# Optimization experiments

Hardware: AMD Instinct MI355X
Metric: run time of the kernel (lower is better)

## Reference

```python
import jax, jax.numpy as jnp
import numpy as np
import math

B, T, E, H = 64, 256, 1024, 16
HD = E // H  # 64
EPS = 1e-5


def layernorm(x, g, b):
    mu = jnp.mean(x, axis=-1, keepdims=True)
    var = jnp.mean(jnp.square(x - mu), axis=-1, keepdims=True)
    return (x - mu) * jax.lax.rsqrt(var + EPS) * g + b


def setup_inputs() -> dict:
    key = jax.random.key(0)
    ks = jax.random.split(key, 10)
    s = 0.02
    return {
        "x": jax.random.normal(ks[0], (B, T, E), dtype=jnp.float32),
        "ln1_g": jnp.ones((E,), jnp.float32),
        "ln1_b": jnp.zeros((E,), jnp.float32),
        "wk": jax.random.normal(ks[1], (H, E, HD), jnp.float32) * s,
        "wq": jax.random.normal(ks[2], (H, E, HD), jnp.float32) * s,
        "wv": jax.random.normal(ks[3], (H, E, HD), jnp.float32) * s,
        "w_proj": jax.random.normal(ks[4], (E, E), jnp.float32) * s,
        "b_proj": jnp.zeros((E,), jnp.float32),
        "ln2_g": jnp.ones((E,), jnp.float32),
        "ln2_b": jnp.zeros((E,), jnp.float32),
        "w1": jax.random.normal(ks[5], (E, E), jnp.float32) * s,
        "b1": jnp.zeros((E,), jnp.float32),
        "w2": jax.random.normal(ks[6], (E, E), jnp.float32) * s,
        "b2": jnp.zeros((E,), jnp.float32),
    }


def reference(x, ln1_g, ln1_b, wk, wq, wv, w_proj, b_proj, ln2_g, ln2_b, w1, b1, w2, b2):
    # --- multi-head causal attention on LN1(x) ---
    h = layernorm(x, ln1_g, ln1_b)
    k = jnp.einsum('bte,hed->bhtd', h, wk)
    q = jnp.einsum('bte,hed->bhtd', h, wq)
    v = jnp.einsum('bte,hed->bhtd', h, wv)
    # NOTE: original computes k @ q^T (K.Q^T), not the standard Q.K^T -- kept faithful
    scores = jnp.einsum('bhtd,bhsd->bhts', k, q) / math.sqrt(HD)
    mask = jnp.tril(jnp.ones((T, T), dtype=bool))
    scores = jnp.where(mask, scores, -jnp.inf)
    attn_w = jax.nn.softmax(scores, axis=-1)  # dropout = identity in eval
    attn = jnp.einsum('bhts,bhsd->bhtd', attn_w, v)
    attn = attn.transpose(0, 2, 1, 3).reshape(B, T, E)  # concat heads
    x = x + attn @ w_proj + b_proj
    # --- feed-forward on LN2(x) ---
    h2 = layernorm(x, ln2_g, ln2_b)
    ff = jax.nn.relu(h2 @ w1 + b1) @ w2 + b2
    return x + ff
```

## Files before the change

kernel.cpp:

```cpp
#include <hip/hip_runtime.h>

typedef unsigned int u32;
typedef unsigned short u16;
typedef __attribute__((ext_vector_type(8))) short bf16x8;
typedef __attribute__((ext_vector_type(4))) float f32x4;

#define GLOBAL_AS __attribute__((address_space(1)))
#define LDS_AS    __attribute__((address_space(3)))

#define B_   64
#define T_   256
#define E_   1024
#define H_   16
#define HD_  64
#define NTOK (B_*T_)
#define K_   1024
#define LNEPS 1e-5f

__device__ __forceinline__ float bflo(u32 u){ return __uint_as_float(u << 16); }
__device__ __forceinline__ float bfhi(u32 u){ return __uint_as_float(u & 0xffff0000u); }
__device__ __forceinline__ u16 f2bf(float f){
  u32 x = __float_as_uint(f);
  u32 r = x + 0x7fffu + ((x >> 16) & 1u);
  return (u16)(r >> 16);
}
__device__ __forceinline__ u16 f2bf_trunc(float f){
  return (u16)(__float_as_uint(f) >> 16);
}
__device__ __forceinline__ u32 pack2(float a, float b){
  return (u32)f2bf(a) | ((u32)f2bf(b) << 16);
}

__device__ __forceinline__ void gload16(const u16* g, u16* l){
  __builtin_amdgcn_global_load_lds((const GLOBAL_AS void*)g, (LDS_AS void*)l, 16, 0, 0);
}

__global__ __launch_bounds__(256) void ln_bf16_kernel(
    const float* __restrict__ x, const float* __restrict__ g,
    const float* __restrict__ b, u16* __restrict__ o)
{
  int lane  = threadIdx.x & 63;
  int token = (blockIdx.x << 2) + (threadIdx.x >> 6);
  const float4* xr = (const float4*)(x + (size_t)token * E_);
  float4 v[4];
  float s = 0.f, ss = 0.f;
  #pragma unroll
  for (int i = 0; i < 4; ++i){
    v[i] = xr[lane + 64 * i];
    s += v[i].x + v[i].y + v[i].z + v[i].w;
    ss = fmaf(v[i].x, v[i].x, fmaf(v[i].y, v[i].y,
         fmaf(v[i].z, v[i].z, fmaf(v[i].w, v[i].w, ss))));
  }
  #pragma unroll
  for (int off = 32; off > 0; off >>= 1){
    s  += __shfl_xor(s,  off);
    ss += __shfl_xor(ss, off);
  }
  float mu   = s * (1.f / E_);
  float var  = ss * (1.f / E_) - mu * mu;
  float rstd = rsqrtf(var + LNEPS);
  const float4* gr = (const float4*)g;
  const float4* br = (const float4*)b;
  uint2* orow = (uint2*)(o + (size_t)token * E_);
  #pragma unroll
  for (int i = 0; i < 4; ++i){
    float4 gg = gr[lane + 64 * i], bb = br[lane + 64 * i];
    float y0 = (v[i].x - mu) * rstd * gg.x + bb.x;
    float y1 = (v[i].y - mu) * rstd * gg.y + bb.y;
    float y2 = (v[i].z - mu) * rstd * gg.z + bb.z;
    float y3 = (v[i].w - mu) * rstd * gg.w + bb.w;
    orow[lane + 64 * i] = make_uint2(pack2(y0, y1), pack2(y2, y3));
  }
}

__global__ __launch_bounds__(256) void convq_kernel(
    const float* __restrict__ wk, const float* __restrict__ wq,
    const float* __restrict__ wv, u16* __restrict__ o)
{
  __shared__ float tile[64 * 68];
  const int zh = blockIdx.x, z = zh >> 4, h = zh & 15;
  const int e0 = blockIdx.y << 6;
  const float* w = (z == 0 ? wk : z == 1 ? wq : wv) + (size_t)h * (E_ * HD_);
  const int t = threadIdx.x;
  {
    int er = t >> 2, d0 = (t & 3) << 4;
    const float4* src = (const float4*)(w + (size_t)(e0 + er) * HD_ + d0);
    #pragma unroll
    for (int i = 0; i < 4; ++i)
      *(float4*)(tile + er * 68 + d0 + 4 * i) = src[i];
  }
  __syncthreads();
  {
    int dr = t >> 2, ee = (t & 3) << 4;
    u32 wd[8];
    #pragma unroll
    for (int j = 0; j < 8; ++j)
      wd[j] = pack2(tile[(ee + 2*j) * 68 + dr], tile[(ee + 2*j + 1) * 68 + dr]);
    u16* dst = o + (size_t)(z * 1024 + h * 64 + dr) * K_ + e0 + ee;
    *(uint4*)(dst    ) = make_uint4(wd[0], wd[1], wd[2], wd[3]);
    *(uint4*)(dst + 8) = make_uint4(wd[4], wd[5], wd[6], wd[7]);
  }
}

__global__ __launch_bounds__(256) void convt_kernel(
    const float* __restrict__ w, u16* __restrict__ o)
{
  __shared__ float tile[64 * 68];
  const int n0 = blockIdx.x << 6, k0 = blockIdx.y << 6;
  const int t = threadIdx.x;
  {
    int kr = t >> 2, nn = (t & 3) << 4;
    const float4* src = (const float4*)(w + (size_t)(k0 + kr) * E_ + n0 + nn);
    #pragma unroll
    for (int i = 0; i < 4; ++i)
      *(float4*)(tile + kr * 68 + nn + 4 * i) = src[i];
  }
  __syncthreads();
  {
    int nr = t >> 2, kk = (t & 3) << 4;
    u32 wd[8];
    #pragma unroll
    for (int j = 0; j < 8; ++j)
      wd[j] = pack2(tile[(kk + 2*j) * 68 + nr], tile[(kk + 2*j + 1) * 68 + nr]);
    u16* dst = o + (size_t)(n0 + nr) * K_ + k0 + kk;
    *(uint4*)(dst    ) = make_uint4(wd[0], wd[1], wd[2], wd[3]);
    *(uint4*)(dst + 8) = make_uint4(wd[4], wd[5], wd[6], wd[7]);
  }
}

#define MF4(I, AV)                                                                 \
  acc[I][0] = __builtin_amdgcn_mfma_f32_16x16x32_bf16(AV, b0, acc[I][0], 0, 0, 0); \
  acc[I][1] = __builtin_amdgcn_mfma_f32_16x16x32_bf16(AV, b1, acc[I][1], 0, 0, 0); \
  acc[I][2] = __builtin_amdgcn_mfma_f32_16x16x32_bf16(AV, b2, acc[I][2], 0, 0, 0); \
  acc[I][3] = __builtin_amdgcn_mfma_f32_16x16x32_bf16(AV, b3, acc[I][3], 0, 0, 0);

#define MG_SLICE(SLOT, DSTSLOT, KOFF, DO_STAGE, VM)                           \
  {                                                                           \
    const u16* As_ = lds + (SLOT) * 16384;                                    \
    const u16* Bs_ = As_ + 8192;                                              \
    u16* dst_ = lds + (DSTSLOT) * 16384;                                      \
    bf16x8 b0 = *(const bf16x8*)(Bs_ + boff);                                 \
    bf16x8 b1 = *(const bf16x8*)(Bs_ + boff + 512);                           \
    bf16x8 b2 = *(const bf16x8*)(Bs_ + boff + 1024);                          \
    bf16x8 b3 = *(const bf16x8*)(Bs_ + boff + 1536);                          \
    bf16x8 a0 = *(const bf16x8*)(As_ + aoff);                                 \
    bf16x8 a1 = *(const bf16x8*)(As_ + aoff + 512);                           \
    bf16x8 a2 = *(const bf16x8*)(As_ + aoff + 1024);                          \
    bf16x8 a3 = *(const bf16x8*)(As_ + aoff + 1536);                          \
    if (DO_STAGE) {                                                           \
      gload16(Ag0 + (KOFF), dst_ + tid * 8);                                  \
      gload16(Ag1 + (KOFF), dst_ + 4096 + tid * 8);                           \
    }                                                                         \
    __builtin_amdgcn_s_barrier();                                             \
    asm volatile("s_waitcnt lgkmcnt(0)" ::: "memory");                        \
    __builtin_amdgcn_sched_barrier(0);                                        \
    __builtin_amdgcn_s_setprio(1);                                            \
    MF4(0, a0) MF4(1, a1) MF4(2, a2) MF4(3, a3)                               \
    __builtin_amdgcn_s_setprio(0);                                            \
    __builtin_amdgcn_s_barrier();                                             \
    asm volatile("" ::: "memory");                                            \
    a0 = *(const bf16x8*)(As_ + aoff + 2048);                                 \
    a1 = *(const bf16x8*)(As_ + aoff + 2560);                                 \
    a2 = *(const bf16x8*)(As_ + aoff + 3072);                                 \
    a3 = *(const bf16x8*)(As_ + aoff + 3584);                                 \
    if (DO_STAGE) {                                                           \
      gload16(Bg0 + (KOFF), dst_ + 8192 + tid * 8);                           \
      gload16(Bg1 + (KOFF), dst_ + 12288 + tid * 8);                          \
    }                                                                         \
    __builtin_amdgcn_s_barrier();                                             \
    asm volatile("s_waitcnt lgkmcnt(0)" ::: "memory");                        \
    __builtin_amdgcn_sched_barrier(0);                                        \
    __builtin_amdgcn_s_setprio(1);                                            \
    MF4(4, a0) MF4(5, a1) MF4(6, a2) MF4(7, a3)                               \
    __builtin_amdgcn_s_setprio(0);                                            \
    VM;                                                                       \
    __builtin_amdgcn_s_barrier();                                             \
    asm volatile("" ::: "memory");                                            \
  }

template<int MODE>
__global__ __launch_bounds__(512, 2) void mgemm_kernel(
    const u16* __restrict__ A, const u16* __restrict__ Bt,
    const float* __restrict__ bias, const float* __restrict__ resid,
    float* __restrict__ Cf, u16* __restrict__ Cb, u16* __restrict__ Cb2)
{
  __shared__ __align__(16) u16 lds[65536];

  const int tid = threadIdx.x, lane = tid & 63, wid = tid >> 6;
  const int wm = wid >> 2, wn = wid & 3;
  const int l15 = lane & 15, quad = lane >> 4;

  const int nwg = (int)(gridDim.x * gridDim.y);
  int wg = (int)(blockIdx.y * gridDim.x + blockIdx.x);
  wg = (wg & 7) * (nwg >> 3) + (wg >> 3);
  const int row0 = (wg & 63) << 8;
  const int col0 = (wg >> 6) << 8;

  const int srow = tid >> 2;
  const int slog = (tid & 3) ^ ((srow + (srow >> 2)) & 3);
  const u16* Ag0 = A  + (size_t)(row0 + srow) * K_ + slog * 8;
  const u16* Ag1 = Ag0 + (size_t)128 * K_;
  const u16* Bg0 = Bt + (size_t)(col0 + srow) * K_ + slog * 8;
  const u16* Bg1 = Bg0 + (size_t)128 * K_;

  const int cofs = ((quad ^ ((l15 + (l15 >> 2)) & 3)) << 3);
  const int aoff = (wm * 128 + l15) * 32 + cofs;
  const int boff = (wn * 64  + l15) * 32 + cofs;

  f32x4 acc[8][4];
  #pragma unroll
  for (int i = 0; i < 8; ++i)
    #pragma unroll
    for (int j = 0; j < 4; ++j)
      acc[i][j] = (f32x4){0.f, 0.f, 0.f, 0.f};

  #pragma unroll
  for (int t = 0; t < 3; ++t) {
    u16* dst = lds + t * 16384;
    gload16(Ag0 + t * 32, dst + tid * 8);
    gload16(Ag1 + t * 32, dst + 4096 + tid * 8);
    gload16(Bg0 + t * 32, dst + 8192 + tid * 8);
    gload16(Bg1 + t * 32, dst + 12288 + tid * 8);
  }
  asm volatile("s_waitcnt vmcnt(8)" ::: "memory");
  __builtin_amdgcn_s_barrier();
  asm volatile("" ::: "memory");

  #pragma unroll 1
  for (int s = 0; s < 29; ++s)
    MG_SLICE(s & 3, (s + 3) & 3, (s + 3) * 32, 1,
             asm volatile("s_waitcnt vmcnt(8)" ::: "memory"))
  MG_SLICE(1, 0, 0, 0, asm volatile("s_waitcnt vmcnt(4)" ::: "memory"))
  MG_SLICE(2, 0, 0, 0, asm volatile("s_waitcnt vmcnt(0)" ::: "memory"))
  MG_SLICE(3, 0, 0, 0, ((void)0))

  if (MODE == 1 || MODE == 3) {
    const int rbase = row0 + wm * 128;
    #pragma unroll
    for (int j = 0; j < 4; ++j) {
      const int n = col0 + wn * 64 + j * 16 + l15;
      const float bn = bias[n];
      #pragma unroll
      for (int i = 0; i < 8; ++i)
        #pragma unroll
        for (int r = 0; r < 4; ++r) {
          const int row = rbase + i * 16 + quad * 4 + r;
          const size_t idx = (size_t)row * E_ + n;
          float v = acc[i][j][r] + bn;
          if (MODE == 1) Cf[idx] = v + resid[idx];
          else           Cf[idx] = v + Cf[idx];
        }
    }
    return;
  }

  u16* ep = lds + wid * 8192;
  const int nb0 = col0 + wn * 64;

  if (MODE == 2) {
    #pragma unroll
    for (int j = 0; j < 4; ++j) {
      const float bn = bias[nb0 + j * 16 + l15];
      #pragma unroll
      for (int i = 0; i < 8; ++i)
        #pragma unroll
        for (int r = 0; r < 4; ++r)
          ep[(i*16 + quad*4 + r) * 64 + j*16 + l15] =
              f2bf(fmaxf(acc[i][j][r] + bn, 0.f));
    }
    __syncthreads();
    const int rbase = row0 + wm * 128;
    #pragma unroll
    for (int it = 0; it < 16; ++it) {
      const int tl = it * 8 + (lane >> 3), c = lane & 7;
      uint4 v = *(const uint4*)(ep + tl * 64 + c * 8);
      *(uint4*)(Cb + (size_t)(rbase + tl) * E_ + nb0 + c * 8) = v;
    }
    return;
  }

  const int z = nb0 >> 10, hh = (nb0 >> 6) & 15;
  const int rows0 = row0 + wm * 128;
  const int bb = rows0 >> 8, tb0 = rows0 & 255;
  if (z < 2) {
    #pragma unroll
    for (int i = 0; i < 8; ++i)
      #pragma unroll
      for (int j = 0; j < 4; ++j)
        #pragma unroll
        for (int r = 0; r < 4; ++r)
          ep[(i*16 + quad*4 + r) * 64 + j*16 + l15] = f2bf(acc[i][j][r]);
    __syncthreads();
    u16* out = (z == 0 ? Cb : Cb2) + ((size_t)(bb * H_ + hh) * T_ + tb0) * HD_;
    #pragma unroll
    for (int it = 0; it < 16; ++it) {
      const int tl = it * 8 + (lane >> 3), c = lane & 7;
      uint4 v = *(const uint4*)(ep + tl * 64 + c * 8);
      *(uint4*)(out + (size_t)tl * HD_ + c * 8) = v;
    }
  } else {
    #pragma unroll
    for (int i = 0; i < 8; ++i)
      #pragma unroll
      for (int j = 0; j < 4; ++j)
        #pragma unroll
        for (int r = 0; r < 4; ++r) {
          const int tl = i*16 + quad*4 + r, d = j*16 + l15;
          const int phys = (tl >> 3) ^ (d & 15);
          ep[d * 128 + phys * 8 + (tl & 7)] = f2bf(acc[i][j][r]);
        }
    __syncthreads();
    u16* out = (u16*)Cf + ((size_t)(bb * H_ + hh) * HD_) * T_;
    #pragma unroll
    for (int it = 0; it < 16; ++it) {
      const int d = it * 4 + (lane >> 4), c = lane & 15;
      const int phys = c ^ (d & 15);
      uint4 v = *(const uint4*)(ep + d * 128 + phys * 8);
      *(uint4*)(out + (size_t)d * T_ + tb0 + c * 8) = v;
    }
  }
}

__global__ __launch_bounds__(256) void fattn_kernel(
    const u16* __restrict__ kk_, const u16* __restrict__ qq_,
    const u16* __restrict__ vt_, u16* __restrict__ out)
{
  __shared__ __align__(16) u16 Pb[4][64 * 72];
  const int tid = threadIdx.x, lane = tid & 63, wv = tid >> 6;
  const int bh = blockIdx.x * 4 + wv;
  const int tblk = blockIdx.y;
  const int l15 = lane & 15, quad = lane >> 4;
  const u16* kb  = kk_ + (size_t)bh * (T_ * HD_);
  const u16* qb  = qq_ + (size_t)bh * (T_ * HD_);
  const u16* vtb = vt_ + (size_t)bh * (HD_ * T_);
  u16* Pw = Pb[wv];

  bf16x8 kf[4][2];
  #pragma unroll
  for (int i = 0; i < 4; ++i)
    #pragma unroll
    for (int c = 0; c < 2; ++c)
      kf[i][c] = *(const bf16x8*)(kb + (size_t)(tblk*64 + i*16 + l15) * HD_ + c*32 + quad*8);

  f32x4 o[4][4];
  float mrow[4][4], lrow[4][4];
  #pragma unroll
  for (int i = 0; i < 4; ++i) {
    #pragma unroll
    for (int j = 0; j < 4; ++j) o[i][j] = (f32x4){0.f, 0.f, 0.f, 0.f};
    #pragma unroll
    for (int r = 0; r < 4; ++r) { mrow[i][r] = -1e30f; lrow[i][r] = 0.f; }
  }

  for (int sb = 0; sb <= tblk; ++sb) {
    f32x4 S[4][4];
    #pragma unroll
    for (int j = 0; j < 4; ++j) {
      bf16x8 qf0 = *(const bf16x8*)(qb + (size_t)(sb*64 + j*16 + l15) * HD_ +      quad*8);
      bf16x8 qf1 = *(const bf16x8*)(qb + (size_t)(sb*64 + j*16 + l15) * HD_ + 32 + quad*8);
      #pragma unroll
      for (int i = 0; i < 4; ++i) {
        f32x4 t0 = __builtin_amdgcn_mfma_f32_16x16x32_bf16(kf[i][0], qf0,
                       (f32x4){0.f,0.f,0.f,0.f}, 0, 0, 0);
        S[i][j] = __builtin_amdgcn_mfma_f32_16x16x32_bf16(kf[i][1], qf1, t0, 0, 0, 0);
      }
    }
    #pragma unroll
    for (int i = 0; i < 4; ++i)
      #pragma unroll
      for (int j = 0; j < 4; ++j)
        #pragma unroll
        for (int r = 0; r < 4; ++r) {
          float val = S[i][j][r] * 0.125f;
          if (sb == tblk) {
            int tl = i*16 + quad*4 + r, sl = j*16 + l15;
            if (sl > tl) val = -1e30f;
          }
          S[i][j][r] = val;
        }
    #pragma unroll
    for (int i = 0; i < 4; ++i)
      #pragma unroll
      for (int r = 0; r < 4; ++r) {
        float mx = fmaxf(fmaxf(S[i][0][r], S[i][1][r]), fmaxf(S[i][2][r], S[i][3][r]));
        #pragma unroll
        for (int msk = 1; msk < 16; msk <<= 1) mx = fmaxf(mx, __shfl_xor(mx, msk));
        float mn = fmaxf(mrow[i][r], mx);
        float al = __expf(mrow[i][r] - mn);
        mrow[i][r] = mn;
        float sm = 0.f;
        #pragma unroll
        for (int j = 0; j < 4; ++j) {
          float p = __expf(S[i][j][r] - mn);
          S[i][j][r] = p;
          sm += p;
        }
        #pragma unroll
        for (int msk = 1; msk < 16; msk <<= 1) sm += __shfl_xor(sm, msk);
        lrow[i][r] = lrow[i][r] * al + sm;
        #pragma unroll
        for (int jd = 0; jd < 4; ++jd) o[i][jd][r] *= al;
      }
    #pragma unroll
    for (int i = 0; i < 4; ++i)
      #pragma unroll
      for (int j = 0; j < 4; ++j)
        #pragma unroll
        for (int r = 0; r < 4; ++r)
          Pw[(i*16 + quad*4 + r) * 72 + j*16 + l15] = f2bf_trunc(S[i][j][r]);
    __syncthreads();
    bf16x8 pf[4][2];
    #pragma unroll
    for (int i = 0; i < 4; ++i)
      #pragma unroll
      for (int c = 0; c < 2; ++c)
        pf[i][c] = *(const bf16x8*)(Pw + (i*16 + l15) * 72 + c*32 + quad*8);
    #pragma unroll
    for (int jd = 0; jd < 4; ++jd) {
      bf16x8 vf0 = *(const bf16x8*)(vtb + (size_t)(jd*16 + l15) * T_ + sb*64 +      quad*8);
      bf16x8 vf1 = *(const bf16x8*)(vtb + (size_t)(jd*16 + l15) * T_ + sb*64 + 32 + quad*8);
      #pragma unroll
      for (int i = 0; i < 4; ++i) {
        f32x4 t0 = __builtin_amdgcn_mfma_f32_16x16x32_bf16(pf[i][0], vf0, o[i][jd], 0, 0, 0);
        o[i][jd] = __builtin_amdgcn_mfma_f32_16x16x32_bf16(pf[i][1], vf1, t0, 0, 0, 0);
      }
    }
    __syncthreads();
  }

  #pragma unroll
  for (int i = 0; i < 4; ++i)
    #pragma unroll
    for (int r = 0; r < 4; ++r) {
      float inv = 1.0f / lrow[i][r];
      #pragma unroll
      for (int jd = 0; jd < 4; ++jd)
        Pw[(i*16 + quad*4 + r) * 72 + jd*16 + l15] = f2bf(o[i][jd][r] * inv);
    }
  __syncthreads();
  {
    const int b = bh >> 4, h = bh & 15;
    const uint4* pr = (const uint4*)(Pw + lane * 72);
    uint4* og = (uint4*)(out + ((size_t)(b * T_ + tblk*64 + lane)) * E_ + h * HD_);
    #pragma unroll
    for (int k = 0; k < 8; ++k) og[k] = pr[k];
  }
}

extern "C" void kernel_launch(void* const* d_in, const int* in_sizes, int n_in,
                              void* d_out, int out_size, void* d_ws, size_t ws_size,
                              hipStream_t stream) {
  const float* x     = (const float*)d_in[0];
  const float* ln1g  = (const float*)d_in[1];
  const float* ln1b  = (const float*)d_in[2];
  const float* wk    = (const float*)d_in[3];
  const float* wq    = (const float*)d_in[4];
  const float* wv    = (const float*)d_in[5];
  const float* wproj = (const float*)d_in[6];
  const float* bproj = (const float*)d_in[7];
  const float* ln2g  = (const float*)d_in[8];
  const float* ln2b  = (const float*)d_in[9];
  const float* w1    = (const float*)d_in[10];
  const float* b1    = (const float*)d_in[11];
  const float* w2    = (const float*)d_in[12];
  const float* b2    = (const float*)d_in[13];
  float* outp = (float*)d_out;

  char* ws = (char*)d_ws;
  const size_t MB = 1024 * 1024;
  u16* wqkvT  = (u16*)(ws);
  u16* wprojT = (u16*)(ws + 6 * MB);
  u16* w1T    = (u16*)(ws + 8 * MB);
  u16* w2T    = (u16*)(ws + 10 * MB);
  u16* hb     = (u16*)(ws + 16 * MB);
  u16* kbuf   = (u16*)(ws + 48 * MB);
  u16* qbuf   = (u16*)(ws + 80 * MB);
  u16* vtbuf  = (u16*)d_out;

  convq_kernel<<<dim3(48, 16), 256, 0, stream>>>(wk, wq, wv, wqkvT);
  convt_kernel<<<dim3(16, 16), 256, 0, stream>>>(wproj, wprojT);
  convt_kernel<<<dim3(16, 16), 256, 0, stream>>>(w1, w1T);
  convt_kernel<<<dim3(16, 16), 256, 0, stream>>>(w2, w2T);

  ln_bf16_kernel<<<NTOK/4, 256, 0, stream>>>(x, ln1g, ln1b, hb);
  mgemm_kernel<0><<<dim3(64, 12), 512, 0, stream>>>(
      hb, wqkvT, nullptr, nullptr, (float*)vtbuf, kbuf, qbuf);
  fattn_kernel<<<dim3(B_*H_/4, 4), 256, 0, stream>>>(kbuf, qbuf, vtbuf, hb);
  mgemm_kernel<1><<<dim3(64, 4), 512, 0, stream>>>(
      hb, wprojT, bproj, x, outp, nullptr, nullptr);
  ln_bf16_kernel<<<NTOK/4, 256, 0, stream>>>(outp, ln2g, ln2b, kbuf);
  mgemm_kernel<2><<<dim3(64, 4), 512, 0, stream>>>(
      kbuf, w1T, b1, nullptr, nullptr, qbuf, nullptr);
  mgemm_kernel<3><<<dim3(64, 4), 512, 0, stream>>>(
      qbuf, w2T, b2, nullptr, outp, nullptr, nullptr);
}
```

Before: 545.0 us.

## Pre-swizzle weights into MFMA fragment layout and load B directly to registers

The weight conversion kernels now write transposed bf16 weights in a blocked layout that matches the per-lane MFMA B-operand fragments. The GEMM loads B fragments straight from global memory into registers, double-buffered across even and odd slices, so only A is staged through LDS. This halves LDS traffic and removes one barrier per slice. The A staging swizzle and the XCD-aware block mapping are also rewritten. In exchange, B is read from global per wave without LDS sharing, and the register pressure and vmcnt accounting get tighter.

```diff
diff --git a/kernel.cpp b/kernel.cpp
--- a/kernel.cpp
+++ b/kernel.cpp
@@ -17,8 +17,6 @@
 #define K_   1024
 #define LNEPS 1e-5f
 
-__device__ __forceinline__ float bflo(u32 u){ return __uint_as_float(u << 16); }
-__device__ __forceinline__ float bfhi(u32 u){ return __uint_as_float(u & 0xffff0000u); }
 __device__ __forceinline__ u16 f2bf(float f){
   u32 x = __float_as_uint(f);
   u32 r = x + 0x7fffu + ((x >> 16) & 1u);
@@ -79,26 +77,32 @@
 {
   __shared__ float tile[64 * 68];
   const int zh = blockIdx.x, z = zh >> 4, h = zh & 15;
-  const int e0 = blockIdx.y << 6;
+  const int k0 = blockIdx.y << 6;
   const float* w = (z == 0 ? wk : z == 1 ? wq : wv) + (size_t)h * (E_ * HD_);
   const int t = threadIdx.x;
   {
-    int er = t >> 2, d0 = (t & 3) << 4;
-    const float4* src = (const float4*)(w + (size_t)(e0 + er) * HD_ + d0);
+    int kr = t >> 2, d0 = (t & 3) << 4;
+    const float4* src = (const float4*)(w + (size_t)(k0 + kr) * HD_ + d0);
     #pragma unroll
     for (int i = 0; i < 4; ++i)
-      *(float4*)(tile + er * 68 + d0 + 4 * i) = src[i];
+      *(float4*)(tile + kr * 68 + d0 + 4 * i) = src[i];
   }
   __syncthreads();
   {
-    int dr = t >> 2, ee = (t & 3) << 4;
-    u32 wd[8];
-    #pragma unroll
-    for (int j = 0; j < 8; ++j)
-      wd[j] = pack2(tile[(ee + 2*j) * 68 + dr], tile[(ee + 2*j + 1) * 68 + dr]);
-    u16* dst = o + (size_t)(z * 1024 + h * 64 + dr) * K_ + e0 + ee;
-    *(uint4*)(dst    ) = make_uint4(wd[0], wd[1], wd[2], wd[3]);
-    *(uint4*)(dst + 8) = make_uint4(wd[4], wd[5], wd[6], wd[7]);
+    const size_t nb32 = (size_t)zh * 32 + (k0 >> 5);
+    #pragma unroll
+    for (int u = 0; u < 2; ++u) {
+      int cid = t * 2 + u;
+      int dd = cid >> 3, kc = cid & 7;
+      u32 wd[4];
+      #pragma unroll
+      for (int e2 = 0; e2 < 4; ++e2)
+        wd[e2] = pack2(tile[(kc * 8 + 2 * e2) * 68 + dd],
+                       tile[(kc * 8 + 2 * e2 + 1) * 68 + dd]);
+      u16* dst = o + (nb32 + (kc >> 2)) * 2048 + (size_t)(dd >> 4) * 512
+                   + (size_t)(((kc & 3) << 4) + (dd & 15)) * 8;
+      *(uint4*)dst = make_uint4(wd[0], wd[1], wd[2], wd[3]);
+    }
   }
 }
 
@@ -117,66 +121,72 @@
   }
   __syncthreads();
   {
-    int nr = t >> 2, kk = (t & 3) << 4;
-    u32 wd[8];
-    #pragma unroll
-    for (int j = 0; j < 8; ++j)
-      wd[j] = pack2(tile[(kk + 2*j) * 68 + nr], tile[(kk + 2*j + 1) * 68 + nr]);
-    u16* dst = o + (size_t)(n0 + nr) * K_ + k0 + kk;
-    *(uint4*)(dst    ) = make_uint4(wd[0], wd[1], wd[2], wd[3]);
-    *(uint4*)(dst + 8) = make_uint4(wd[4], wd[5], wd[6], wd[7]);
-  }
-}
-
-#define MF4(I, AV)                                                                 \
-  acc[I][0] = __builtin_amdgcn_mfma_f32_16x16x32_bf16(AV, b0, acc[I][0], 0, 0, 0); \
-  acc[I][1] = __builtin_amdgcn_mfma_f32_16x16x32_bf16(AV, b1, acc[I][1], 0, 0, 0); \
-  acc[I][2] = __builtin_amdgcn_mfma_f32_16x16x32_bf16(AV, b2, acc[I][2], 0, 0, 0); \
-  acc[I][3] = __builtin_amdgcn_mfma_f32_16x16x32_bf16(AV, b3, acc[I][3], 0, 0, 0);
-
-#define MG_SLICE(SLOT, DSTSLOT, KOFF, DO_STAGE, VM)                           \
-  {                                                                           \
-    const u16* As_ = lds + (SLOT) * 16384;                                    \
-    const u16* Bs_ = As_ + 8192;                                              \
-    u16* dst_ = lds + (DSTSLOT) * 16384;                                      \
-    bf16x8 b0 = *(const bf16x8*)(Bs_ + boff);                                 \
-    bf16x8 b1 = *(const bf16x8*)(Bs_ + boff + 512);                           \
-    bf16x8 b2 = *(const bf16x8*)(Bs_ + boff + 1024);                          \
-    bf16x8 b3 = *(const bf16x8*)(Bs_ + boff + 1536);                          \
-    bf16x8 a0 = *(const bf16x8*)(As_ + aoff);                                 \
-    bf16x8 a1 = *(const bf16x8*)(As_ + aoff + 512);                           \
-    bf16x8 a2 = *(const bf16x8*)(As_ + aoff + 1024);                          \
-    bf16x8 a3 = *(const bf16x8*)(As_ + aoff + 1536);                          \
+    const size_t nb32 = (size_t)(n0 >> 6) * 32 + (k0 >> 5);
+    #pragma unroll
+    for (int u = 0; u < 2; ++u) {
+      int cid = t * 2 + u;
+      int dd = cid >> 3, kc = cid & 7;
+      u32 wd[4];
+      #pragma unroll
+      for (int e2 = 0; e2 < 4; ++e2)
+        wd[e2] = pack2(tile[(kc * 8 + 2 * e2) * 68 + dd],
+                       tile[(kc * 8 + 2 * e2 + 1) * 68 + dd]);
+      u16* dst = o + (nb32 + (kc >> 2)) * 2048 + (size_t)(dd >> 4) * 512
+                   + (size_t)(((kc & 3) << 4) + (dd & 15)) * 8;
+      *(uint4*)dst = make_uint4(wd[0], wd[1], wd[2], wd[3]);
+    }
+  }
+}
+
+#define MF4(I, AV, BV)                                                               \
+  acc[I][0] = __builtin_amdgcn_mfma_f32_16x16x32_bf16(AV, BV[0], acc[I][0], 0, 0, 0);\
+  acc[I][1] = __builtin_amdgcn_mfma_f32_16x16x32_bf16(AV, BV[1], acc[I][1], 0, 0, 0);\
+  acc[I][2] = __builtin_amdgcn_mfma_f32_16x16x32_bf16(AV, BV[2], acc[I][2], 0, 0, 0);\
+  acc[I][3] = __builtin_amdgcn_mfma_f32_16x16x32_bf16(AV, BV[3], acc[I][3], 0, 0, 0);
+
+#define BLOADS(BV, SS) {                                                      \
+    const u16* bp_ = Bp + (size_t)(SS) * 2048;                                \
+    BV[0] = *(const bf16x8*)(bp_);                                            \
+    BV[1] = *(const bf16x8*)(bp_ + 512);                                      \
+    BV[2] = *(const bf16x8*)(bp_ + 1024);                                     \
+    BV[3] = *(const bf16x8*)(bp_ + 1536);                                     \
+  }
+
+#define MSLICE(SLOT, DST, KA, DO_STAGE, BV, BL, VM) {                         \
+    const u16* As_ = lds + (SLOT) * 8192;                                     \
+    bf16x8 a0 = *(const bf16x8*)(As_ + aoffb);                                \
+    bf16x8 a1 = *(const bf16x8*)(As_ + aoffb + 512);                          \
+    bf16x8 a2 = *(const bf16x8*)(As_ + aoffb + 1024);                         \
+    bf16x8 a3 = *(const bf16x8*)(As_ + aoffb + 1536);                         \
     if (DO_STAGE) {                                                           \
-      gload16(Ag0 + (KOFF), dst_ + tid * 8);                                  \
-      gload16(Ag1 + (KOFF), dst_ + 4096 + tid * 8);                           \
+      u16* d_ = lds + (DST) * 8192;                                           \
+      gload16(Ag0 + (KA), d_ + tid * 8);                                      \
+      gload16(Ag1 + (KA), d_ + 4096 + tid * 8);                               \
     }                                                                         \
     __builtin_amdgcn_s_barrier();                                             \
     asm volatile("s_waitcnt lgkmcnt(0)" ::: "memory");                        \
     __builtin_amdgcn_sched_barrier(0);                                        \
     __builtin_amdgcn_s_setprio(1);                                            \
-    MF4(0, a0) MF4(1, a1) MF4(2, a2) MF4(3, a3)                               \
+    MF4(0, a0, BV) MF4(1, a1, BV) MF4(2, a2, BV) MF4(3, a3, BV)               \
     __builtin_amdgcn_s_setprio(0);                                            \
-    __builtin_amdgcn_s_barrier();                                             \
-    asm volatile("" ::: "memory");                                            \
-    a0 = *(const bf16x8*)(As_ + aoff + 2048);                                 \
-    a1 = *(const bf16x8*)(As_ + aoff + 2560);                                 \
-    a2 = *(const bf16x8*)(As_ + aoff + 3072);                                 \
-    a3 = *(const bf16x8*)(As_ + aoff + 3584);                                 \
-    if (DO_STAGE) {                                                           \
-      gload16(Bg0 + (KOFF), dst_ + 8192 + tid * 8);                           \
-      gload16(Bg1 + (KOFF), dst_ + 12288 + tid * 8);                          \
-    }                                                                         \
-    __builtin_amdgcn_s_barrier();                                             \
+    a0 = *(const bf16x8*)(As_ + aoffb + 2048);                                \
+    a1 = *(const bf16x8*)(As_ + aoffb + 2560);                                \
+    a2 = *(const bf16x8*)(As_ + aoffb + 3072);                                \
+    a3 = *(const bf16x8*)(As_ + aoffb + 3584);                                \
     asm volatile("s_waitcnt lgkmcnt(0)" ::: "memory");                        \
     __builtin_amdgcn_sched_barrier(0);                                        \
     __builtin_amdgcn_s_setprio(1);                                            \
-    MF4(4, a0) MF4(5, a1) MF4(6, a2) MF4(7, a3)                               \
+    MF4(4, a0, BV) MF4(5, a1, BV) MF4(6, a2, BV) MF4(7, a3, BV)               \
     __builtin_amdgcn_s_setprio(0);                                            \
+    BL;                                                                       \
     VM;                                                                       \
     __builtin_amdgcn_s_barrier();                                             \
     asm volatile("" ::: "memory");                                            \
   }
+
+#define VM12 asm volatile("s_waitcnt vmcnt(12)" ::: "memory")
+#define VM10 asm volatile("s_waitcnt vmcnt(10)" ::: "memory")
+#define VM8  asm volatile("s_waitcnt vmcnt(8)"  ::: "memory")
 
 template<int MODE>
 __global__ __launch_bounds__(512, 2) void mgemm_kernel(
@@ -190,22 +200,22 @@
   const int wm = wid >> 2, wn = wid & 3;
   const int l15 = lane & 15, quad = lane >> 4;
 
-  const int nwg = (int)(gridDim.x * gridDim.y);
-  int wg = (int)(blockIdx.y * gridDim.x + blockIdx.x);
-  wg = (wg & 7) * (nwg >> 3) + (wg >> 3);
-  const int row0 = (wg & 63) << 8;
-  const int col0 = (wg >> 6) << 8;
-
-  const int srow = tid >> 2;
-  const int slog = (tid & 3) ^ ((srow + (srow >> 2)) & 3);
-  const u16* Ag0 = A  + (size_t)(row0 + srow) * K_ + slog * 8;
+  const int b = (int)blockIdx.x;
+  const int xcd = b & 7, ib = b >> 3;
+  const int row0 = ((xcd << 3) + (ib & 7)) << 8;
+  const int col0 = (ib >> 3) << 8;
+
+  const int sc   = (tid & 7) ^ ((tid >> 3) & 7);
+  const int srow = 2 * (tid >> 3) + (sc >> 2);
+  const int skof = (sc & 3) << 3;
+  const u16* Ag0 = A + (size_t)(row0 + srow) * K_ + skof;
   const u16* Ag1 = Ag0 + (size_t)128 * K_;
-  const u16* Bg0 = Bt + (size_t)(col0 + srow) * K_ + slog * 8;
-  const u16* Bg1 = Bg0 + (size_t)128 * K_;
-
-  const int cofs = ((quad ^ ((l15 + (l15 >> 2)) & 3)) << 3);
-  const int aoff = (wm * 128 + l15) * 32 + cofs;
-  const int boff = (wn * 64  + l15) * 32 + cofs;
+
+  const int rhalf = l15 >> 1;
+  const int cph   = ((((l15 & 1) << 2) | quad) ^ rhalf);
+  const int aoffb = wm * 4096 + rhalf * 64 + cph * 8;
+
+  const u16* Bp = Bt + (size_t)((col0 >> 6) + wn) * 65536 + lane * 8;
 
   f32x4 acc[8][4];
   #pragma unroll
@@ -214,25 +224,29 @@
     for (int j = 0; j < 4; ++j)
       acc[i][j] = (f32x4){0.f, 0.f, 0.f, 0.f};
 
-  #pragma unroll
-  for (int t = 0; t < 3; ++t) {
-    u16* dst = lds + t * 16384;
-    gload16(Ag0 + t * 32, dst + tid * 8);
-    gload16(Ag1 + t * 32, dst + 4096 + tid * 8);
-    gload16(Bg0 + t * 32, dst + 8192 + tid * 8);
-    gload16(Bg1 + t * 32, dst + 12288 + tid * 8);
-  }
-  asm volatile("s_waitcnt vmcnt(8)" ::: "memory");
+  bf16x8 bE[4], bO[4];
+
+  #pragma unroll
+  for (int t3 = 0; t3 < 3; ++t3) {
+    u16* d_ = lds + t3 * 8192;
+    gload16(Ag0 + t3 * 32, d_ + tid * 8);
+    gload16(Ag1 + t3 * 32, d_ + 4096 + tid * 8);
+  }
+  BLOADS(bE, 0)
+  BLOADS(bO, 1)
+  asm volatile("s_waitcnt vmcnt(12)" ::: "memory");
   __builtin_amdgcn_s_barrier();
   asm volatile("" ::: "memory");
 
   #pragma unroll 1
-  for (int s = 0; s < 29; ++s)
-    MG_SLICE(s & 3, (s + 3) & 3, (s + 3) * 32, 1,
-             asm volatile("s_waitcnt vmcnt(8)" ::: "memory"))
-  MG_SLICE(1, 0, 0, 0, asm volatile("s_waitcnt vmcnt(4)" ::: "memory"))
-  MG_SLICE(2, 0, 0, 0, asm volatile("s_waitcnt vmcnt(0)" ::: "memory"))
-  MG_SLICE(3, 0, 0, 0, ((void)0))
+  for (int s = 0; s < 28; s += 2) {
+    MSLICE(s & 3, (s + 3) & 3, (s + 3) * 32, 1, bE, BLOADS(bE, s + 2), VM12)
+    MSLICE((s + 1) & 3, (s + 4) & 3, (s + 4) * 32, 1, bO, BLOADS(bO, s + 3), VM12)
+  }
+  MSLICE(0, 3, 31 * 32, 1, bE, BLOADS(bE, 30), VM12)
+  MSLICE(1, 0, 0,       0, bO, BLOADS(bO, 31), VM10)
+  MSLICE(2, 0, 0,       0, bE, (void)0,        VM8 )
+  MSLICE(3, 0, 0,       0, bO, (void)0,        (void)0)
 
   if (MODE == 1 || MODE == 3) {
     const int rbase = row0 + wm * 128;
@@ -483,14 +497,14 @@
   convt_kernel<<<dim3(16, 16), 256, 0, stream>>>(w2, w2T);
 
   ln_bf16_kernel<<<NTOK/4, 256, 0, stream>>>(x, ln1g, ln1b, hb);
-  mgemm_kernel<0><<<dim3(64, 12), 512, 0, stream>>>(
+  mgemm_kernel<0><<<768, 512, 0, stream>>>(
       hb, wqkvT, nullptr, nullptr, (float*)vtbuf, kbuf, qbuf);
   fattn_kernel<<<dim3(B_*H_/4, 4), 256, 0, stream>>>(kbuf, qbuf, vtbuf, hb);
-  mgemm_kernel<1><<<dim3(64, 4), 512, 0, stream>>>(
+  mgemm_kernel<1><<<256, 512, 0, stream>>>(
       hb, wprojT, bproj, x, outp, nullptr, nullptr);
   ln_bf16_kernel<<<NTOK/4, 256, 0, stream>>>(outp, ln2g, ln2b, kbuf);
-  mgemm_kernel<2><<<dim3(64, 4), 512, 0, stream>>>(
+  mgemm_kernel<2><<<256, 512, 0, stream>>>(
       kbuf, w1T, b1, nullptr, nullptr, qbuf, nullptr);
-  mgemm_kernel<3><<<dim3(64, 4), 512, 0, stream>>>(
+  mgemm_kernel<3><<<256, 512, 0, stream>>>(
       qbuf, w2T, b2, nullptr, outp, nullptr, nullptr);
 }
```

Result: faster. 527.0 us (-3.3%).
